# Optimization experiments

Measured on AMD Instinct MI355X. Metric: run time of the kernel, lower is better.

The kernel has to match this reference:

```python
import jax, jax.numpy as jnp
import numpy as np
from jax import lax

N, H, W, T = 8, 100, 152, 256
STRIDE = 8
ANCHOR_SIZE = 64.0
PRE_NMS_THRESH = 0.05
PRE_NMS_TOP_N = 1000
NMS_THRESH = 0.6
POST_TOP_N = 100
IMG_H, IMG_W = 800, 1216
BW = (10.0, 10.0, 5.0, 5.0)          # BoxCoder weights (wx, wy, ww, wh)
DWH_CLIP = float(np.log(1000.0 / 16.0))
TO_REMOVE = 1.0


def setup_inputs() -> dict:
    key = jax.random.key(0)
    k1, k2, k3 = jax.random.split(key, 3)
    box_regression = jax.random.normal(k1, (N, 4, H, W), dtype=jnp.float32)
    centerness = jax.random.normal(k2, (N, 1, H, W), dtype=jnp.float32)
    dot_product_logits = jax.random.normal(k3, (N, H * W, T), dtype=jnp.float32)
    # anchor grid matching permute_and_flatten's (H, W, A) row-major ordering
    ys, xs = jnp.meshgrid(jnp.arange(H, dtype=jnp.float32),
                          jnp.arange(W, dtype=jnp.float32), indexing="ij")
    cx = xs.reshape(-1) * STRIDE + STRIDE / 2.0
    cy = ys.reshape(-1) * STRIDE + STRIDE / 2.0
    half = ANCHOR_SIZE / 2.0
    anc = jnp.stack([cx - half, cy - half, cx + half, cy + half], axis=-1)  # [H*W, 4]
    anchors = jnp.broadcast_to(anc, (N, H * W, 4)).astype(jnp.float32)
    return {"box_regression": box_regression, "centerness": centerness,
            "anchors": anchors, "dot_product_logits": dot_product_logits}


def _decode(rel, anc):
    w = anc[..., 2] - anc[..., 0] + TO_REMOVE
    h = anc[..., 3] - anc[..., 1] + TO_REMOVE
    cx = anc[..., 0] + 0.5 * w
    cy = anc[..., 1] + 0.5 * h
    dx = rel[..., 0] / BW[0]
    dy = rel[..., 1] / BW[1]
    dw = jnp.minimum(rel[..., 2] / BW[2], DWH_CLIP)
    dh = jnp.minimum(rel[..., 3] / BW[3], DWH_CLIP)
    pcx = dx * w + cx
    pcy = dy * h + cy
    pw = jnp.exp(dw) * w
    ph = jnp.exp(dh) * h
    return jnp.stack([pcx - 0.5 * pw, pcy - 0.5 * ph,
                      pcx + 0.5 * pw - 1.0, pcy + 0.5 * ph - 1.0], axis=-1)


def _iou_one_vs_all(box, boxes):
    area1 = (box[2] - box[0] + TO_REMOVE) * (box[3] - box[1] + TO_REMOVE)
    area2 = (boxes[:, 2] - boxes[:, 0] + TO_REMOVE) * (boxes[:, 3] - boxes[:, 1] + TO_REMOVE)
    lt = jnp.maximum(box[:2], boxes[:, :2])
    rb = jnp.minimum(box[2:], boxes[:, 2:])
    wh = jnp.maximum(rb - lt + TO_REMOVE, 0.0)
    inter = wh[:, 0] * wh[:, 1]
    return inter / (area1 + area2 - inter)


def _nms_single(boxes, scores):
    # greedy NMS, fixed POST_TOP_N iterations (fpn_post_nms_top_n)
    def step(s, _):
        j = jnp.argmax(s)
        sj = s[j]
        bj = boxes[j]
        flag = (sj > 0).astype(boxes.dtype)
        ious = _iou_one_vs_all(bj, boxes)
        s = jnp.where(ious > NMS_THRESH, 0.0, s).at[j].set(0.0)
        return s, (bj * flag, sj * flag)
    _, (kb, ks) = lax.scan(step, scores, None, length=POST_TOP_N)
    return kb, ks


def reference(box_regression, centerness, anchors, dot_product_logits):
    n, _, h, w = box_regression.shape
    # sigmoid + MEAN token aggregation  -> [N, HWA]
    scores = jax.nn.sigmoid(dot_product_logits).mean(-1)
    # permute_and_flatten: [N,4A,H,W] -> [N, HWA, 4]
    box_reg = box_regression.reshape(n, 1, 4, h, w).transpose(0, 3, 4, 1, 2).reshape(n, -1, 4)
    ctr = jax.nn.sigmoid(centerness.reshape(n, 1, 1, h, w).transpose(0, 3, 4, 1, 2).reshape(n, -1))
    cand = scores > PRE_NMS_THRESH          # threshold on raw aggregated scores
    cls = scores * ctr                      # centerness-weighted score
    masked = jnp.where(cand, cls, 0.0)
    vals, idx = lax.top_k(masked, PRE_NMS_TOP_N)          # per-image top-k candidates
    valid = jnp.take_along_axis(cand, idx, axis=1)        # [N, PRE_NMS_TOP_N]
    sel_reg = jnp.take_along_axis(box_reg, idx[..., None], axis=1)
    sel_anc = jnp.take_along_axis(anchors, idx[..., None], axis=1)
    boxes = _decode(sel_reg, sel_anc)
    # clip_to_image
    boxes = jnp.stack([
        jnp.clip(boxes[..., 0], 0.0, IMG_W - 1.0),
        jnp.clip(boxes[..., 1], 0.0, IMG_H - 1.0),
        jnp.clip(boxes[..., 2], 0.0, IMG_W - 1.0),
        jnp.clip(boxes[..., 3], 0.0, IMG_H - 1.0)], axis=-1)
    vf = valid.astype(boxes.dtype)
    det_scores = jnp.sqrt(jnp.where(valid, vals, 1.0)) * vf   # sqrt of cls*ctr, safe grad
    keep_boxes, keep_scores = jax.vmap(_nms_single)(boxes, det_scores)
    return keep_boxes, keep_scores
```

## Files before the change

### kernel.cpp

```cpp
#include <hip/hip_runtime.h>
#include <math.h>

#define NN 8
#define HH 100
#define WW 152
#define HW (HH*WW)
#define HWP 15360
#define TT 256
#define TOPN 1000
#define CAP 1024
#define POSTN 100
#define IMGW 1216
#define IMGH 800
#define DWH_CLIP 4.135166556742356f

typedef unsigned long long u64;
typedef unsigned int u32;

__global__ __launch_bounds__(256) void score_kernel(
    const float* __restrict__ logits,
    const float* __restrict__ centerness,
    float* __restrict__ masked)
{
    int wid  = blockIdx.x * 4 + (threadIdx.x >> 6);
    int lane = threadIdx.x & 63;
    const float4 v = *(reinterpret_cast<const float4*>(logits + (size_t)wid * TT) + lane);
    float s = 0.f;
    s += __fdividef(1.f, 1.f + expf(-v.x));
    s += __fdividef(1.f, 1.f + expf(-v.y));
    s += __fdividef(1.f, 1.f + expf(-v.z));
    s += __fdividef(1.f, 1.f + expf(-v.w));
    #pragma unroll
    for (int off = 32; off; off >>= 1) s += __shfl_xor(s, off, 64);
    if (lane == 0) {
        float score = s * (1.0f / 256.0f);
        float c = centerness[wid];
        float ctr = 1.f / (1.f + expf(-c));
        masked[wid] = (score > 0.05f) ? score * ctr : 0.f;
    }
}

__global__ __launch_bounds__(256, 1) void select_nms_kernel(
    const float* __restrict__ masked,
    const float* __restrict__ box_reg,
    float* __restrict__ out)
{
    const int n    = blockIdx.x;
    const int tid  = threadIdx.x;
    const int wv   = tid >> 6;
    const int lane = tid & 63;

    __shared__ __align__(16) u32 lbits[HWP];
    __shared__ u64    keys[CAP];
    __shared__ float4 sbox[CAP];
    __shared__ float  sscr[CAP];
    __shared__ int    parts[2][4];
    __shared__ int    s_cnt1, s_cnt2, s_kept;

    float* outb = out + (size_t)n * POSTN * 4;
    float* outs = out + (size_t)NN * POSTN * 4 + (size_t)n * POSTN;

    {
        const uint4* mb4 = reinterpret_cast<const uint4*>(masked + (size_t)n * HW);
        uint4* lb4 = reinterpret_cast<uint4*>(lbits);
        #pragma unroll
        for (int j = 0; j < HWP / 1024; j++) {
            int f = j * 256 + tid;
            uint4 v = make_uint4(0u, 0u, 0u, 0u);
            if (f < HW / 4) v = mb4[f];
            lb4[f] = v;
        }
    }
    __syncthreads();

    int p = 0;
    u32 lo = 0u, hi = 0x3F800000u;
    u32 thr = 0u;
    bool early = false;
    while (lo < hi) {
        u32 mid = lo + ((hi - lo) >> 1);
        int c = 0;
        const uint4* lb4 = reinterpret_cast<const uint4*>(lbits);
        #pragma unroll
        for (int j = 0; j < HWP / 1024; j++) {
            uint4 v = lb4[j * 256 + tid];
            c += (v.x > mid) + (v.y > mid) + (v.z > mid) + (v.w > mid);
        }
        #pragma unroll
        for (int off = 32; off; off >>= 1) c += __shfl_xor(c, off, 64);
        if (lane == 0) parts[p][wv] = c;
        __syncthreads();
        int tot = parts[p][0] + parts[p][1] + parts[p][2] + parts[p][3];
        p ^= 1;
        if (tot >= TOPN && tot <= CAP) { thr = mid; early = true; break; }
        if (tot <= TOPN - 1) hi = mid; else lo = mid + 1;
    }
    if (!early) thr = lo;

    #pragma unroll
    for (int j = 0; j < CAP / 256; j++) keys[tid + j * 256] = 0ull;
    if (tid == 0) { s_cnt1 = 0; s_cnt2 = 0; }
    __syncthreads();
    {
        const uint4* lb4 = reinterpret_cast<const uint4*>(lbits);
        #pragma unroll
        for (int j = 0; j < HWP / 1024; j++) {
            int f = j * 256 + tid;
            uint4 v = lb4[f];
            int e = f * 4;
            if (v.x > thr) { int q = atomicAdd(&s_cnt1, 1); if (q < CAP) keys[q] = (((u64)v.x) << 32) | (u32)(~(e + 0)); }
            if (v.y > thr) { int q = atomicAdd(&s_cnt1, 1); if (q < CAP) keys[q] = (((u64)v.y) << 32) | (u32)(~(e + 1)); }
            if (v.z > thr) { int q = atomicAdd(&s_cnt1, 1); if (q < CAP) keys[q] = (((u64)v.z) << 32) | (u32)(~(e + 2)); }
            if (v.w > thr) { int q = atomicAdd(&s_cnt1, 1); if (q < CAP) keys[q] = (((u64)v.w) << 32) | (u32)(~(e + 3)); }
        }
    }
    __syncthreads();
    if (!early && thr > 0u) {
        const int c1 = min(s_cnt1, TOPN);
        const uint4* lb4 = reinterpret_cast<const uint4*>(lbits);
        #pragma unroll
        for (int j = 0; j < HWP / 1024; j++) {
            int f = j * 256 + tid;
            uint4 v = lb4[f];
            int e = f * 4;
            if (v.x == thr) { int q = atomicAdd(&s_cnt2, 1); if (c1 + q < TOPN) keys[c1 + q] = (((u64)thr) << 32) | (u32)(~(e + 0)); }
            if (v.y == thr) { int q = atomicAdd(&s_cnt2, 1); if (c1 + q < TOPN) keys[c1 + q] = (((u64)thr) << 32) | (u32)(~(e + 1)); }
            if (v.z == thr) { int q = atomicAdd(&s_cnt2, 1); if (c1 + q < TOPN) keys[c1 + q] = (((u64)thr) << 32) | (u32)(~(e + 2)); }
            if (v.w == thr) { int q = atomicAdd(&s_cnt2, 1); if (c1 + q < TOPN) keys[c1 + q] = (((u64)thr) << 32) | (u32)(~(e + 3)); }
        }
        __syncthreads();
    }
    if (early) __syncthreads();

    for (int k = 2; k <= CAP; k <<= 1) {
        for (int j2 = k >> 1; j2 > 0; j2 >>= 1) {
            #pragma unroll
            for (int e = 0; e < CAP / 256; e++) {
                int i = tid + e * 256;
                int ixj = i ^ j2;
                if (ixj > i) {
                    u64 a = keys[i], bb = keys[ixj];
                    bool sw = ((i & k) == 0) ? (a < bb) : (a > bb);
                    if (sw) { keys[i] = bb; keys[ixj] = a; }
                }
            }
            __syncthreads();
        }
    }
    if (tid < CAP - TOPN) keys[TOPN + tid] = 0ull;
    __syncthreads();

    #pragma unroll
    for (int e = 0; e < CAP / 256; e++) {
        int pos = tid + e * 256;
        u64 kk = keys[pos];
        float s = __uint_as_float((u32)(kk >> 32));
        float4 box = make_float4(0.f, 0.f, 0.f, 0.f);
        if (s > 0.f) {
            int loc = (int)(~(u32)kk);
            float acx = (float)(loc % WW) * 8.f + 4.f;
            float acy = (float)(loc / WW) * 8.f + 4.f;
            float a0 = acx - 32.f, a1 = acy - 32.f, a2 = acx + 32.f, a3 = acy + 32.f;
            float r0 = box_reg[((size_t)n * 4 + 0) * HW + loc];
            float r1 = box_reg[((size_t)n * 4 + 1) * HW + loc];
            float r2 = box_reg[((size_t)n * 4 + 2) * HW + loc];
            float r3 = box_reg[((size_t)n * 4 + 3) * HW + loc];
            float w  = a2 - a0 + 1.0f;
            float h  = a3 - a1 + 1.0f;
            float cx = a0 + 0.5f * w;
            float cy = a1 + 0.5f * h;
            float dx = r0 / 10.0f;
            float dy = r1 / 10.0f;
            float dw = fminf(r2 / 5.0f, DWH_CLIP);
            float dh = fminf(r3 / 5.0f, DWH_CLIP);
            float pcx = dx * w + cx;
            float pcy = dy * h + cy;
            float pw  = expf(dw) * w;
            float ph  = expf(dh) * h;
            float x1 = pcx - 0.5f * pw;
            float y1 = pcy - 0.5f * ph;
            float x2 = pcx + 0.5f * pw - 1.0f;
            float y2 = pcy + 0.5f * ph - 1.0f;
            box.x = fminf(fmaxf(x1, 0.f), (float)(IMGW - 1));
            box.y = fminf(fmaxf(y1, 0.f), (float)(IMGH - 1));
            box.z = fminf(fmaxf(x2, 0.f), (float)(IMGW - 1));
            box.w = fminf(fmaxf(y2, 0.f), (float)(IMGH - 1));
        }
        sbox[pos] = box;
        sscr[pos] = s;
    }
    __syncthreads();

    if (tid < 64) {
        float ax1 = 0.f, ay1 = 0.f, ax2 = 0.f, ay2 = 0.f, aar = 0.f;
        float bx1 = 0.f, by1 = 0.f, bx2 = 0.f, by2 = 0.f, bar = 0.f;
        int  kept = 0;
        bool done = false;
        const double MD = (double)0.6f + 0x1p-25;
        const int pa = lane >> 3, pb = lane & 7;

        for (int i0 = 0; i0 < CAP && !done; i0 += 8) {
            u32 myMask = 0u, dMask = 0u;
            #pragma unroll
            for (int c = 0; c < 8; c++) {
                float  s  = sscr[i0 + c];
                float4 cb = sbox[i0 + c];
                if (s <= 0.f) dMask |= (1u << c);
                float carea = (cb.z - cb.x + 1.f) * (cb.w - cb.y + 1.f);

                float ix1 = fmaxf(cb.x, ax1), iy1 = fmaxf(cb.y, ay1);
                float ix2 = fminf(cb.z, ax2), iy2 = fminf(cb.w, ay2);
                float iw = fmaxf(ix2 - ix1 + 1.f, 0.f), ih = fmaxf(iy2 - iy1 + 1.f, 0.f);
                float interA = iw * ih;
                float denomA = (carea + aar) - interA;
                bool supA = (lane < kept) && ((double)interA > MD * (double)denomA);

                ix1 = fmaxf(cb.x, bx1); iy1 = fmaxf(cb.y, by1);
                ix2 = fminf(cb.z, bx2); iy2 = fminf(cb.w, by2);
                iw = fmaxf(ix2 - ix1 + 1.f, 0.f); ih = fmaxf(iy2 - iy1 + 1.f, 0.f);
                float interB = iw * ih;
                float denomB = (carea + bar) - interB;
                bool supB = (lane < kept - 64) && ((double)interB > MD * (double)denomB);

                if (supA || supB) myMask |= (1u << c);
            }
            #pragma unroll
            for (int off = 32; off; off >>= 1) myMask |= __shfl_xor(myMask, off, 64);

            bool psup = false;
            if (pa < pb) {
                float4 A = sbox[i0 + pa];
                float4 B = sbox[i0 + pb];
                float areaA = (A.z - A.x + 1.f) * (A.w - A.y + 1.f);
                float areaB = (B.z - B.x + 1.f) * (B.w - B.y + 1.f);
                float ix1 = fmaxf(A.x, B.x), iy1 = fmaxf(A.y, B.y);
                float ix2 = fminf(A.z, B.z), iy2 = fminf(A.w, B.w);
                float iw = fmaxf(ix2 - ix1 + 1.f, 0.f), ih = fmaxf(iy2 - iy1 + 1.f, 0.f);
                float inter = iw * ih;
                float denom = (areaA + areaB) - inter;
                psup = ((double)inter > MD * (double)denom);
            }
            u64 P = __ballot(psup);

            u64 kbytes = 0ull;
            for (int c = 0; c < 8; c++) {
                if ((dMask >> c) & 1u) { done = true; break; }
                u32 sup = (myMask >> c) & 1u;
                u64 col = (P >> c) & 0x0101010101010101ull;
                if (col & kbytes) sup = 1u;
                if (!sup) {
                    float4 cb = sbox[i0 + c];
                    float  s  = sscr[i0 + c];
                    float carea = (cb.z - cb.x + 1.f) * (cb.w - cb.y + 1.f);
                    if (kept < 64) {
                        if (lane == kept)      { ax1 = cb.x; ay1 = cb.y; ax2 = cb.z; ay2 = cb.w; aar = carea; }
                    } else {
                        if (lane == kept - 64) { bx1 = cb.x; by1 = cb.y; bx2 = cb.z; by2 = cb.w; bar = carea; }
                    }
                    if (lane == 0) {
                        outb[kept * 4 + 0] = cb.x; outb[kept * 4 + 1] = cb.y;
                        outb[kept * 4 + 2] = cb.z; outb[kept * 4 + 3] = cb.w;
                        outs[kept] = sqrtf(s);
                    }
                    kbytes |= 1ull << (8 * c);
                    ++kept;
                    if (kept == POSTN) { done = true; break; }
                }
            }
        }
        if (lane == 0) s_kept = kept;
    }
    __syncthreads();

    const int cnt = s_kept;
    for (int i = cnt + tid; i < POSTN; i += 256) {
        outb[i * 4 + 0] = 0.f; outb[i * 4 + 1] = 0.f;
        outb[i * 4 + 2] = 0.f; outb[i * 4 + 3] = 0.f;
        outs[i] = 0.f;
    }
}

extern "C" void kernel_launch(void* const* d_in, const int* in_sizes, int n_in,
                              void* d_out, int out_size, void* d_ws, size_t ws_size,
                              hipStream_t stream) {
    const float* box_reg = (const float*)d_in[0];
    const float* center  = (const float*)d_in[1];
    const float* logits  = (const float*)d_in[3];
    float* out = (float*)d_out;

    float* masked = (float*)d_ws;

    score_kernel<<<(NN * HW) / 4, 256, 0, stream>>>(logits, center, masked);
    select_nms_kernel<<<NN, 256, 0, stream>>>(masked, box_reg, out);
}
```

Baseline: 283.4 us.

## Parallelize NMS across all 256 threads with 16-candidate blocks

```diff
diff --git a/kernel.cpp b/kernel.cpp
--- a/kernel.cpp
+++ b/kernel.cpp
@@ -56,6 +56,11 @@
     __shared__ float  sscr[CAP];
     __shared__ int    parts[2][4];
     __shared__ int    s_cnt1, s_cnt2, s_kept;
+    __shared__ float4 kbox[128];
+    __shared__ float  karea[128];
+    __shared__ u64    s_supw[4];
+    __shared__ u64    s_matw[4];
+    __shared__ int    s_kept2, s_done2;
 
     float* outb = out + (size_t)n * POSTN * 4;
     float* outs = out + (size_t)NN * POSTN * 4 + (size_t)n * POSTN;
@@ -128,9 +133,8 @@
             if (v.z == thr) { int q = atomicAdd(&s_cnt2, 1); if (c1 + q < TOPN) keys[c1 + q] = (((u64)thr) << 32) | (u32)(~(e + 2)); }
             if (v.w == thr) { int q = atomicAdd(&s_cnt2, 1); if (c1 + q < TOPN) keys[c1 + q] = (((u64)thr) << 32) | (u32)(~(e + 3)); }
         }
-        __syncthreads();
-    }
-    if (early) __syncthreads();
+    }
+    __syncthreads();
 
     for (int k = 2; k <= CAP; k <<= 1) {
         for (int j2 = k >> 1; j2 > 0; j2 >>= 1) {
@@ -189,86 +193,82 @@
         sbox[pos] = box;
         sscr[pos] = s;
     }
-    __syncthreads();
-
-    if (tid < 64) {
-        float ax1 = 0.f, ay1 = 0.f, ax2 = 0.f, ay2 = 0.f, aar = 0.f;
-        float bx1 = 0.f, by1 = 0.f, bx2 = 0.f, by2 = 0.f, bar = 0.f;
-        int  kept = 0;
-        bool done = false;
+    if (tid == 0) { s_kept2 = 0; s_done2 = 0; }
+    __syncthreads();
+
+    {
         const double MD = (double)0.6f + 0x1p-25;
-        const int pa = lane >> 3, pb = lane & 7;
-
-        for (int i0 = 0; i0 < CAP && !done; i0 += 8) {
-            u32 myMask = 0u, dMask = 0u;
+        const int c  = tid >> 4;
+        const int kb = tid & 15;
+        int kept = 0;
+
+        for (int i0 = 0; i0 < CAP; i0 += 16) {
+            float4 cb = sbox[i0 + c];
+            float  ca = (cb.z - cb.x + 1.f) * (cb.w - cb.y + 1.f);
+            bool sup = false;
             #pragma unroll
-            for (int c = 0; c < 8; c++) {
-                float  s  = sscr[i0 + c];
-                float4 cb = sbox[i0 + c];
-                if (s <= 0.f) dMask |= (1u << c);
-                float carea = (cb.z - cb.x + 1.f) * (cb.w - cb.y + 1.f);
-
-                float ix1 = fmaxf(cb.x, ax1), iy1 = fmaxf(cb.y, ay1);
-                float ix2 = fminf(cb.z, ax2), iy2 = fminf(cb.w, ay2);
-                float iw = fmaxf(ix2 - ix1 + 1.f, 0.f), ih = fmaxf(iy2 - iy1 + 1.f, 0.f);
-                float interA = iw * ih;
-                float denomA = (carea + aar) - interA;
-                bool supA = (lane < kept) && ((double)interA > MD * (double)denomA);
-
-                ix1 = fmaxf(cb.x, bx1); iy1 = fmaxf(cb.y, by1);
-                ix2 = fminf(cb.z, bx2); iy2 = fminf(cb.w, by2);
-                iw = fmaxf(ix2 - ix1 + 1.f, 0.f); ih = fmaxf(iy2 - iy1 + 1.f, 0.f);
-                float interB = iw * ih;
-                float denomB = (carea + bar) - interB;
-                bool supB = (lane < kept - 64) && ((double)interB > MD * (double)denomB);
-
-                if (supA || supB) myMask |= (1u << c);
-            }
-            #pragma unroll
-            for (int off = 32; off; off >>= 1) myMask |= __shfl_xor(myMask, off, 64);
-
+            for (int j = 0; j < 8; j++) {
+                int slot = kb + 16 * j;
+                if (slot < kept) {
+                    float4 kx = kbox[slot];
+                    float ix1 = fmaxf(cb.x, kx.x), iy1 = fmaxf(cb.y, kx.y);
+                    float ix2 = fminf(cb.z, kx.z), iy2 = fminf(cb.w, kx.w);
+                    float iw = fmaxf(ix2 - ix1 + 1.f, 0.f), ih = fmaxf(iy2 - iy1 + 1.f, 0.f);
+                    float inter = iw * ih;
+                    float denom = (ca + karea[slot]) - inter;
+                    sup = sup || ((double)inter > MD * (double)denom);
+                }
+            }
             bool psup = false;
-            if (pa < pb) {
-                float4 A = sbox[i0 + pa];
-                float4 B = sbox[i0 + pb];
+            if (kb < c) {
+                float4 A = sbox[i0 + kb];
                 float areaA = (A.z - A.x + 1.f) * (A.w - A.y + 1.f);
-                float areaB = (B.z - B.x + 1.f) * (B.w - B.y + 1.f);
-                float ix1 = fmaxf(A.x, B.x), iy1 = fmaxf(A.y, B.y);
-                float ix2 = fminf(A.z, B.z), iy2 = fminf(A.w, B.w);
+                float ix1 = fmaxf(A.x, cb.x), iy1 = fmaxf(A.y, cb.y);
+                float ix2 = fminf(A.z, cb.z), iy2 = fminf(A.w, cb.w);
                 float iw = fmaxf(ix2 - ix1 + 1.f, 0.f), ih = fmaxf(iy2 - iy1 + 1.f, 0.f);
                 float inter = iw * ih;
-                float denom = (areaA + areaB) - inter;
+                float denom = (areaA + ca) - inter;
                 psup = ((double)inter > MD * (double)denom);
             }
-            u64 P = __ballot(psup);
-
-            u64 kbytes = 0ull;
-            for (int c = 0; c < 8; c++) {
-                if ((dMask >> c) & 1u) { done = true; break; }
-                u32 sup = (myMask >> c) & 1u;
-                u64 col = (P >> c) & 0x0101010101010101ull;
-                if (col & kbytes) sup = 1u;
-                if (!sup) {
-                    float4 cb = sbox[i0 + c];
-                    float  s  = sscr[i0 + c];
-                    float carea = (cb.z - cb.x + 1.f) * (cb.w - cb.y + 1.f);
-                    if (kept < 64) {
-                        if (lane == kept)      { ax1 = cb.x; ay1 = cb.y; ax2 = cb.z; ay2 = cb.w; aar = carea; }
-                    } else {
-                        if (lane == kept - 64) { bx1 = cb.x; by1 = cb.y; bx2 = cb.z; by2 = cb.w; bar = carea; }
+            u64 bs = __ballot(sup);
+            u64 bp = __ballot(psup);
+            if (lane == 0) { s_supw[wv] = bs; s_matw[wv] = bp; }
+            __syncthreads();
+
+            if (tid < 64) {
+                bool dd = (tid < 16) ? (sscr[i0 + tid] <= 0.f) : false;
+                u64 db = __ballot(dd);
+                u32 dead16 = (u32)db & 0xFFFFu;
+                u32 kb16 = 0u;
+                int kk = kept;
+                int dn = 0;
+                for (int cc = 0; cc < 16; cc++) {
+                    if ((dead16 >> cc) & 1u) { dn = 1; break; }
+                    u32 supbits = (u32)(s_supw[cc >> 2] >> ((cc & 3) * 16)) & 0xFFFFu;
+                    u32 colm    = (u32)(s_matw[cc >> 2] >> ((cc & 3) * 16)) & 0xFFFFu;
+                    bool scc = (supbits != 0u) || ((colm & kb16) != 0u);
+                    if (!scc) {
+                        float4 wbx = sbox[i0 + cc];
+                        float  wsc = sscr[i0 + cc];
+                        float  war = (wbx.z - wbx.x + 1.f) * (wbx.w - wbx.y + 1.f);
+                        if (tid == 0) {
+                            kbox[kk] = wbx; karea[kk] = war;
+                            outb[kk * 4 + 0] = wbx.x; outb[kk * 4 + 1] = wbx.y;
+                            outb[kk * 4 + 2] = wbx.z; outb[kk * 4 + 3] = wbx.w;
+                            outs[kk] = sqrtf(wsc);
+                        }
+                        kb16 |= (1u << cc);
+                        ++kk;
+                        if (kk == POSTN) { dn = 1; break; }
                     }
-                    if (lane == 0) {
-                        outb[kept * 4 + 0] = cb.x; outb[kept * 4 + 1] = cb.y;
-                        outb[kept * 4 + 2] = cb.z; outb[kept * 4 + 3] = cb.w;
-                        outs[kept] = sqrtf(s);
-                    }
-                    kbytes |= 1ull << (8 * c);
-                    ++kept;
-                    if (kept == POSTN) { done = true; break; }
                 }
-            }
-        }
-        if (lane == 0) s_kept = kept;
+                if (tid == 0) { s_kept2 = kk; s_done2 = dn; }
+            }
+            __syncthreads();
+            kept = s_kept2;
+            if (s_done2) break;
+        }
+        if (tid == 0) s_kept = kept;
     }
     __syncthreads();
 
```

Result: faster. 270.0 us (-4.7%).
